# Kernel optimization log

Hardware: AMD Instinct MI355X
Metric: run time of the kernel (lower is better)

The kernel has to match this reference:

```python
import jax, jax.numpy as jnp
import numpy as np

EMBED_DIM = 768
NUM_HEADS = 12
LORA_DIM = 64
HEAD_DIM = EMBED_DIM // NUM_HEADS
SCALING = float(HEAD_DIM) ** -0.5


def quick_gelu(x):
    return x * jax.nn.sigmoid(1.702 * x)


def setup_inputs() -> dict:
    key = jax.random.key(0)
    ks = jax.random.split(key, 12)
    bsz, tgt_len, E = 128, 197, EMBED_DIM
    x = jax.random.normal(ks[0], (bsz, tgt_len, E), dtype=jnp.float32)
    attn_mask = jnp.zeros((bsz, tgt_len, tgt_len), dtype=jnp.float32)
    top_idx = jax.random.randint(ks[1], (bsz,), 0, tgt_len)
    s = 0.02
    return {
        "x": x,
        "attn_mask": attn_mask,
        "in_proj_weight": jax.random.normal(ks[2], (3 * E, E)) * s,
        "in_proj_bias": jnp.zeros((3 * E,), jnp.float32),
        "out_proj_weight": jax.random.normal(ks[3], (E, E)) * s,
        "out_proj_bias": jnp.zeros((E,), jnp.float32),
        "lora_a": jax.random.normal(ks[4], (LORA_DIM, E)) * s,
        "lora_b": jax.random.normal(ks[5], (3 * E, LORA_DIM)) * s,
        "down_weight": jax.random.normal(ks[6], (LORA_DIM, E)) * s,
        "down_bias": jax.random.normal(ks[7], (LORA_DIM,)) * 1e-6,
        "up_weight": jax.random.normal(ks[8], (E, LORA_DIM)) * s,
        "up_bias": jnp.zeros((E,), jnp.float32),
        "n_f": 16,
        "top_idx": top_idx,
    }


def reference(x, attn_mask, in_proj_weight, in_proj_bias, out_proj_weight,
              out_proj_bias, lora_a, lora_b, down_weight, down_bias,
              up_weight, up_bias, n_f, top_idx):
    bsz, tgt_len, E = x.shape
    H, hd = NUM_HEADS, HEAD_DIM
    b = bsz // n_f

    # fused QKV + LoRA delta
    qkv = x @ in_proj_weight.T + in_proj_bias          # [bsz, L, 3E]
    qkv = qkv + (x @ lora_a.T) @ lora_b.T              # LoRA delta
    qkv = qkv.reshape(bsz, tgt_len, 3, H, hd)
    qkv = jnp.transpose(qkv, (2, 0, 3, 1, 4))          # [3, bsz, H, L, hd]
    q, k, v = qkv[0], qkv[1], qkv[2]

    # gather per-sample CLS query before scaling (matches torch order)
    q_1 = q[jnp.arange(bsz), :, top_idx, :]            # [bsz, H, hd]
    q_1 = jnp.transpose(q_1.reshape(b, n_f, H, hd), (0, 2, 1, 3))  # [b, H, f, hd]

    # frame-local attention
    attn = jnp.einsum('bhqd,bhkd->bhqk', q * SCALING, k) + attn_mask[:, None, :, :]
    attn = jax.nn.softmax(attn, axis=-1)
    xo = jnp.einsum('bhqk,bhkd->bhqd', attn, v)
    xo = jnp.transpose(xo, (0, 2, 1, 3)).reshape(bsz, tgt_len, E)
    xo = xo @ out_proj_weight.T + out_proj_bias        # [bsz, L, E]

    # global CLS attention over all frames' keys/values
    k_g = jnp.transpose(k.reshape(b, n_f, H, tgt_len, hd), (0, 2, 1, 3, 4)).reshape(b, H, n_f * tgt_len, hd)
    v_g = jnp.transpose(v.reshape(b, n_f, H, tgt_len, hd), (0, 2, 1, 3, 4)).reshape(b, H, n_f * tgt_len, hd)
    mask_g = attn_mask[:, -1, :].reshape(b, n_f * tgt_len)  # [b, f*L]

    attn_1 = jnp.einsum('bhfd,bhkd->bhfk', q_1 * SCALING, k_g) + mask_g[:, None, None, :]
    attn_1 = jax.nn.softmax(attn_1, axis=-1)
    x_1 = jnp.einsum('bhfk,bhkd->bhfd', attn_1, v_g)
    x_1 = jnp.transpose(x_1, (0, 2, 1, 3)).reshape(b, n_f, E)
    x_1 = x_1 @ out_proj_weight.T + out_proj_bias      # [b, f, E]

    # adapter on gathered CLS outputs
    x_0 = xo[jnp.arange(bsz), top_idx, :].reshape(b, n_f, E)
    x_0 = quick_gelu(x_0 @ down_weight.T + down_bias)
    x_0 = x_0 @ up_weight.T + up_bias                  # [b, f, E]

    update_cls = (x_0 + x_1).reshape(bsz, E)
    xo = xo.at[jnp.arange(bsz), top_idx, :].set(update_cls)
    return xo
```

## Files before the change

### kernel.cpp

```cpp
#include <hip/hip_runtime.h>
#include <hip/hip_bf16.h>

typedef __attribute__((ext_vector_type(4))) float f32x4;
typedef __attribute__((ext_vector_type(8))) short s16x8;

#define BSZ 128
#define TGT 197
#define EDIM 768
#define NH 12
#define HD 64
#define NF 16
#define M_TOT (BSZ*TGT)
#define QKV_N (3*EDIM)
#define KG (NF*TGT)
#define VSTR 264
#define NSPL 8
#define KSPL 394
#define LSTR 424

__device__ __forceinline__ float b2f(unsigned short u) {
  return __uint_as_float(((unsigned int)u) << 16);
}
__device__ __forceinline__ float bf2f(__hip_bfloat16 b) { return __bfloat162float(b); }
__device__ __forceinline__ __hip_bfloat16 f2bf(float f) { return __float2bfloat16(f); }
__device__ __forceinline__ unsigned int packbf(float a, float b) {
  __hip_bfloat16 x = __float2bfloat16(a), y = __float2bfloat16(b);
  return (unsigned int)*(unsigned short*)&x | ((unsigned int)*(unsigned short*)&y << 16);
}
__device__ __forceinline__ int swz(int t, int c) {
  return t*64 + (c ^ ((((t & 7) ^ ((t >> 3) & 3))) << 3));
}
__device__ __forceinline__ int vswz(int d, int t) {
  return d*VSTR + (t ^ (d & 56));
}

__device__ __forceinline__ void gload_lds16(const void* gsrc, void* ldst) {
  __builtin_amdgcn_global_load_lds(
      (const __attribute__((address_space(1))) unsigned int*)gsrc,
      (__attribute__((address_space(3))) unsigned int*)ldst, 16, 0, 0);
}

struct CvBatch {
  const void* src[7];
  void* dst[7];
  int off8[8];
};

__global__ __launch_bounds__(256) void prep(
    const void* __restrict__ xsrc, const void* __restrict__ msrc,
    __hip_bfloat16* __restrict__ x_c, __hip_bfloat16* __restrict__ mask_c,
    CvBatch cb, int* __restrict__ flag, unsigned int* __restrict__ mznz)
{
  __shared__ float smax[256];
  const int tid = threadIdx.x;
  const unsigned short* xs = (const unsigned short*)xsrc;
  float mx = 0.f;
  for (int j = tid; j < 1024; j += 256) {
    float v = fabsf(b2f(xs[j]));
    mx = (v < 1e30f) ? fmaxf(mx, v) : 1e30f;
  }
  smax[tid] = mx;
  __syncthreads();
  if (tid == 0) {
    float m = 0.f;
    for (int j = 0; j < 256; ++j) m = fmaxf(m, smax[j]);
    smax[0] = (m < 100.f) ? 1.f : 0.f;
    if (blockIdx.x == 0) *flag = (m < 100.f) ? 1 : 0;
  }
  __syncthreads();
  const int isbf = (int)smax[0];

  const int gsz = gridDim.x * 256;
  const int gi = blockIdx.x * 256 + tid;

  {
    const unsigned int* mw = (const unsigned int*)msrc;
    const int nwords = isbf ? (4967552/2) : 4967552;
    const unsigned int am = isbf ? 0x7fff7fffu : 0x7fffffffu;
    unsigned int acc = 0;
    for (int i = gi; i < nwords; i += gsz) acc |= (mw[i] & am);
    if (acc) atomicOr(mznz, 1u);
  }

  {
    const int total = cb.off8[7];
    for (int i = gi; i < total; i += gsz) {
      int s = 0;
      #pragma unroll
      for (int k = 1; k < 7; ++k) s += (i >= cb.off8[k]);
      const int li = i - cb.off8[s];
      if (isbf) {
        ((s16x8*)cb.dst[s])[li] = ((const s16x8*)cb.src[s])[li];
      } else {
        const f32x4* sp = (const f32x4*)cb.src[s];
        f32x4 a = sp[li*2], b = sp[li*2+1];
        s16x8 o;
        #pragma unroll
        for (int j = 0; j < 4; ++j) { __hip_bfloat16 t = f2bf(a[j]); o[j] = *(short*)&t; }
        #pragma unroll
        for (int j = 0; j < 4; ++j) { __hip_bfloat16 t = f2bf(b[j]); o[4+j] = *(short*)&t; }
        ((s16x8*)cb.dst[s])[li] = o;
      }
    }
  }

  if (!isbf) {
    {
      const f32x4* s = (const f32x4*)xsrc;
      s16x8* d = (s16x8*)x_c;
      for (int i = gi; i < 19365888/8; i += gsz) {
        f32x4 a = s[i*2], b = s[i*2+1];
        s16x8 o;
        #pragma unroll
        for (int j = 0; j < 4; ++j) { __hip_bfloat16 t = f2bf(a[j]); o[j] = *(short*)&t; }
        #pragma unroll
        for (int j = 0; j < 4; ++j) { __hip_bfloat16 t = f2bf(b[j]); o[4+j] = *(short*)&t; }
        d[i] = o;
      }
    }
    {
      const f32x4* s = (const f32x4*)msrc;
      s16x8* d = (s16x8*)mask_c;
      for (int i = gi; i < 4967552/8; i += gsz) {
        f32x4 a = s[i*2], b = s[i*2+1];
        s16x8 o;
        #pragma unroll
        for (int j = 0; j < 4; ++j) { __hip_bfloat16 t = f2bf(a[j]); o[j] = *(short*)&t; }
        #pragma unroll
        for (int j = 0; j < 4; ++j) { __hip_bfloat16 t = f2bf(b[j]); o[4+j] = *(short*)&t; }
        d[i] = o;
      }
    }
  }
}

__global__ __launch_bounds__(256) void build_wc(
    const void* __restrict__ W,
    const void* __restrict__ la,
    const void* __restrict__ lb,
    __hip_bfloat16* __restrict__ Wc,
    const int* __restrict__ flag)
{
  __shared__ float lbr[64];
  const int isbf = *flag;
  const int n = blockIdx.x;
  if (threadIdx.x < 64)
    lbr[threadIdx.x] = isbf ? bf2f(((const __hip_bfloat16*)lb)[n*64 + threadIdx.x])
                            : ((const float*)lb)[n*64 + threadIdx.x];
  __syncthreads();
  if (isbf) {
    const __hip_bfloat16* Wb = (const __hip_bfloat16*)W;
    const __hip_bfloat16* lab = (const __hip_bfloat16*)la;
    for (int e = threadIdx.x; e < EDIM; e += 256) {
      float acc = bf2f(Wb[(size_t)n*EDIM + e]);
      for (int r = 0; r < 64; ++r) acc += lbr[r] * bf2f(lab[r*EDIM + e]);
      Wc[(size_t)n*EDIM + e] = f2bf(acc);
    }
  } else {
    const float* Wf = (const float*)W;
    const float* laf = (const float*)la;
    for (int e = threadIdx.x; e < EDIM; e += 256) {
      float acc = Wf[(size_t)n*EDIM + e];
      for (int r = 0; r < 64; ++r) acc += lbr[r] * laf[r*EDIM + e];
      Wc[(size_t)n*EDIM + e] = f2bf(acc);
    }
  }
}

__global__ __launch_bounds__(512) void gemm_bt_8ph(
    const __hip_bfloat16* __restrict__ A,
    const __hip_bfloat16* __restrict__ A_alt,
    const __hip_bfloat16* __restrict__ B,
    const __hip_bfloat16* __restrict__ bias,
    void* __restrict__ C,
    int M, int N, int K, int ntiles,
    const int* __restrict__ flag, int flag_mode)
{
  __shared__ char lds[131072];
  const int tid = threadIdx.x;
  const int wave = tid >> 6, lane = tid & 63;
  const int l16 = lane & 15, kq = lane >> 4;
  const int wr = wave >> 2, wc2 = wave & 3;

  const int nwg = gridDim.x;
  const int bid = blockIdx.x;
  const int qc = nwg >> 3, rc = nwg & 7;
  const int xcd = bid & 7;
  const int wgid = (xcd < rc ? xcd*(qc+1) : rc*(qc+1) + (xcd-rc)*qc) + (bid >> 3);
  const long brow = (long)(wgid / ntiles) * 256;
  const long bcol = (long)(wgid % ntiles) * 256;

  const int isbf = *flag;
  const __hip_bfloat16* Ause = isbf ? A_alt : A;
  const int nkt = K >> 6;

  const int srow = tid >> 3;
  const int schunk = tid & 7;
  const int wuni = wave << 10;

  auto stA = [&](int t, int buf, int issue) {
    int ar = issue*64 + srow;
    int cs = schunk ^ (ar & 7);
    long gr = brow + ar; if (gr > (long)M - 1) gr = M - 1;
    gload_lds16(Ause + gr*(long)K + t*64 + cs*8,
                lds + buf*65536 + issue*8192 + wuni);
  };
  auto stB = [&](int t, int buf, int issue) {
    int br = issue*64 + srow;
    int cs = schunk ^ (br & 7);
    gload_lds16(B + (bcol + br)*(long)K + t*64 + cs*8,
                lds + buf*65536 + 32768 + issue*8192 + wuni);
  };
  auto rdA = [&](int buf, int q, int a, int ks) -> s16x8 {
    int ar = wr*128 + q*32 + a*16 + l16;
    int ch = ks*4 + kq;
    return *(const s16x8*)(lds + buf*65536 + ar*128 + ((ch ^ (ar & 7)) << 4));
  };
  auto rdB = [&](int buf, int ni, int ks) -> s16x8 {
    int br = wc2*64 + ni*16 + l16;
    int ch = ks*4 + kq;
    return *(const s16x8*)(lds + buf*65536 + 32768 + br*128 + ((ch ^ (br & 7)) << 4));
  };

  f32x4 acc[8][4];
  #pragma unroll
  for (int i = 0; i < 8; ++i)
    #pragma unroll
    for (int j = 0; j < 4; ++j) acc[i][j] = (f32x4){0.f,0.f,0.f,0.f};

  stB(0,0,0); stB(0,0,1); stB(0,0,2); stB(0,0,3);
  stA(0,0,0); stA(0,0,2); stA(0,0,1); stA(0,0,3);
  asm volatile("s_waitcnt vmcnt(2)" ::: "memory");
  __builtin_amdgcn_s_barrier();

  for (int t = 0; t < nkt; ++t) {
    const int cur = t & 1, nxt = cur ^ 1;
    const bool pf = (t + 1 < nkt);
    s16x8 bfr[4][2], af[2][2];

    #pragma unroll
    for (int ni = 0; ni < 4; ++ni) { bfr[ni][0] = rdB(cur,ni,0); bfr[ni][1] = rdB(cur,ni,1); }
    af[0][0]=rdA(cur,0,0,0); af[0][1]=rdA(cur,0,0,1);
    af[1][0]=rdA(cur,0,1,0); af[1][1]=rdA(cur,0,1,1);
    if (pf) { stB(t+1,nxt,0); stB(t+1,nxt,1); }
    __builtin_amdgcn_s_barrier();
    asm volatile("s_waitcnt lgkmcnt(0)" ::: "memory");
    __builtin_amdgcn_sched_barrier(0);
    __builtin_amdgcn_s_setprio(1);
    #pragma unroll
    for (int ks = 0; ks < 2; ++ks)
      #pragma unroll
      for (int ni = 0; ni < 4; ++ni) {
        acc[0][ni] = __builtin_amdgcn_mfma_f32_16x16x32_bf16(af[0][ks], bfr[ni][ks], acc[0][ni], 0,0,0);
        acc[1][ni] = __builtin_amdgcn_mfma_f32_16x16x32_bf16(af[1][ks], bfr[ni][ks], acc[1][ni], 0,0,0);
      }
    __builtin_amdgcn_s_setprio(0);

    af[0][0]=rdA(cur,1,0,0); af[0][1]=rdA(cur,1,0,1);
    af[1][0]=rdA(cur,1,1,0); af[1][1]=rdA(cur,1,1,1);
    if (pf) {
      stB(t+1,nxt,2); stB(t+1,nxt,3);
      asm volatile("s_waitcnt vmcnt(4)" ::: "memory");
    } else {
      asm volatile("s_waitcnt vmcnt(0)" ::: "memory");
    }
    __builtin_amdgcn_s_barrier();
    asm volatile("s_waitcnt lgkmcnt(0)" ::: "memory");
    __builtin_amdgcn_sched_barrier(0);
    __builtin_amdgcn_s_setprio(1);
    #pragma unroll
    for (int ks = 0; ks < 2; ++ks)
      #pragma unroll
      for (int ni = 0; ni < 4; ++ni) {
        acc[2][ni] = __builtin_amdgcn_mfma_f32_16x16x32_bf16(af[0][ks], bfr[ni][ks], acc[2][ni], 0,0,0);
        acc[3][ni] = __builtin_amdgcn_mfma_f32_16x16x32_bf16(af[1][ks], bfr[ni][ks], acc[3][ni], 0,0,0);
      }
    __builtin_amdgcn_s_setprio(0);

    af[0][0]=rdA(cur,2,0,0); af[0][1]=rdA(cur,2,0,1);
    af[1][0]=rdA(cur,2,1,0); af[1][1]=rdA(cur,2,1,1);
    if (pf) { stA(t+1,nxt,0); stA(t+1,nxt,2); }
    __builtin_amdgcn_s_barrier();
    asm volatile("s_waitcnt lgkmcnt(0)" ::: "memory");
    __builtin_amdgcn_sched_barrier(0);
    __builtin_amdgcn_s_setprio(1);
    #pragma unroll
    for (int ks = 0; ks < 2; ++ks)
      #pragma unroll
      for (int ni = 0; ni < 4; ++ni) {
        acc[4][ni] = __builtin_amdgcn_mfma_f32_16x16x32_bf16(af[0][ks], bfr[ni][ks], acc[4][ni], 0,0,0);
        acc[5][ni] = __builtin_amdgcn_mfma_f32_16x16x32_bf16(af[1][ks], bfr[ni][ks], acc[5][ni], 0,0,0);
      }
    __builtin_amdgcn_s_setprio(0);

    af[0][0]=rdA(cur,3,0,0); af[0][1]=rdA(cur,3,0,1);
    af[1][0]=rdA(cur,3,1,0); af[1][1]=rdA(cur,3,1,1);
    if (pf) { stA(t+1,nxt,1); stA(t+1,nxt,3); }
    asm volatile("s_waitcnt vmcnt(2)" ::: "memory");
    __builtin_amdgcn_s_barrier();
    asm volatile("s_waitcnt lgkmcnt(0)" ::: "memory");
    __builtin_amdgcn_sched_barrier(0);
    __builtin_amdgcn_s_setprio(1);
    #pragma unroll
    for (int ks = 0; ks < 2; ++ks)
      #pragma unroll
      for (int ni = 0; ni < 4; ++ni) {
        acc[6][ni] = __builtin_amdgcn_mfma_f32_16x16x32_bf16(af[0][ks], bfr[ni][ks], acc[6][ni], 0,0,0);
        acc[7][ni] = __builtin_amdgcn_mfma_f32_16x16x32_bf16(af[1][ks], bfr[ni][ks], acc[7][ni], 0,0,0);
      }
    __builtin_amdgcn_s_setprio(0);
  }

  __builtin_amdgcn_s_barrier();

  const int f32o = flag_mode && (!isbf);
  float bv[4];
  #pragma unroll
  for (int ni = 0; ni < 4; ++ni) bv[ni] = bf2f(bias[bcol + wc2*64 + ni*16 + l16]);
  const int o4 = kq*4;

  if (!f32o) {
    __hip_bfloat16* eb = (__hip_bfloat16*)(lds + wave*2048);
    __hip_bfloat16* Cb = (__hip_bfloat16*)C;
    const int rr = lane >> 3, cg = lane & 7;
    #pragma unroll
    for (int mi = 0; mi < 8; ++mi) {
      #pragma unroll
      for (int ni = 0; ni < 4; ++ni)
        #pragma unroll
        for (int r = 0; r < 4; ++r) {
          const int row16 = o4 + r;
          const int sidx = row16*64 + ((((ni*2 + (l16 >> 3)) ^ (row16 & 7)) << 3) | (l16 & 7));
          eb[sidx] = f2bf(acc[mi][ni][r] + bv[ni]);
        }
      asm volatile("s_waitcnt lgkmcnt(0)" ::: "memory");
      __builtin_amdgcn_sched_barrier(0);
      #pragma unroll
      for (int pass = 0; pass < 2; ++pass) {
        const int row16 = pass*8 + rr;
        const long grow = brow + wr*128 + mi*16 + row16;
        if (grow < M) {
          s16x8 v = *(const s16x8*)(eb + row16*64 + ((cg ^ (row16 & 7)) << 3));
          *(s16x8*)(Cb + grow*(long)N + bcol + wc2*64 + cg*8) = v;
        }
      }
      asm volatile("s_waitcnt lgkmcnt(0)" ::: "memory");
      __builtin_amdgcn_sched_barrier(0);
    }
  } else {
    #pragma unroll
    for (int mi = 0; mi < 8; ++mi)
      #pragma unroll
      for (int ni = 0; ni < 4; ++ni)
        #pragma unroll
        for (int r = 0; r < 4; ++r) {
          const long grow = brow + wr*128 + mi*16 + o4 + r;
          if (grow < M)
            ((float*)C)[grow*(long)N + bcol + wc2*64 + ni*16 + l16] = acc[mi][ni][r] + bv[ni];
        }
  }
}

__global__ __launch_bounds__(256) void attn_fused(
    const __hip_bfloat16* __restrict__ qkv,
    const __hip_bfloat16* __restrict__ mask,
    const __hip_bfloat16* __restrict__ mask_raw,
    const int* __restrict__ flag,
    const unsigned int* __restrict__ mzp,
    __hip_bfloat16* __restrict__ xop)
{
  __shared__ __hip_bfloat16 lVt[64*VSTR];

  const int tid = threadIdx.x;
  const int blk = blockIdx.x;
  const int xcd = blk & 7;
  const int slot = blk >> 3;
  const int ih = xcd * 192 + (slot >> 2);
  const int qt = slot & 3;
  const int h = ih % NH;
  const int i = ih / NH;
  const int q0 = qt * 64;
  const size_t rowbase = (size_t)i * TGT;
  const int wave = tid >> 6, lane = tid & 63;
  const int l16 = lane & 15, kq = lane >> 4;
  const int mz = (*mzp == 0u);
  const __hip_bfloat16* msk = (*flag) ? mask_raw : mask;

  int qr = q0 + wave*16 + l16;
  const int qrc = qr > TGT-1 ? TGT-1 : qr;
  s16x8 qf[2];
  #pragma unroll
  for (int kk = 0; kk < 2; ++kk)
    qf[kk] = *(const s16x8*)(qkv + (rowbase + qrc)*QKV_N + h*HD + kk*32 + kq*8);

  const f32x4 z = {0.f,0.f,0.f,0.f};
  for (int idx = tid; idx < 224*8; idx += 256) {
    int t = idx >> 3, c8 = idx & 7;
    f32x4 vv = z;
    if (t < TGT) vv = *(const f32x4*)(qkv + (rowbase + t)*QKV_N + 2*EDIM + h*HD + c8*8);
    const __hip_bfloat16* pv = (const __hip_bfloat16*)&vv;
    const int tx = t ^ (c8 << 3);
    #pragma unroll
    for (int j = 0; j < 8; ++j)
      lVt[(c8*8 + j)*VSTR + tx] = pv[j];
  }
  __syncthreads();

  f32x4 acc[14];
  #pragma unroll
  for (int nf = 0; nf < 14; ++nf) {
    int trow = nf*16 + l16; if (trow > TGT-1) trow = TGT-1;
    acc[nf] = (f32x4){0.f,0.f,0.f,0.f};
    #pragma unroll
    for (int kk = 0; kk < 2; ++kk) {
      s16x8 kf = *(const s16x8*)(qkv + (rowbase + trow)*QKV_N + EDIM + h*HD + kk*32 + kq*8);
      acc[nf] = __builtin_amdgcn_mfma_f32_16x16x32_bf16(kf, qf[kk], acc[nf], 0, 0, 0);
    }
  }

  float mx = -1e30f;
  #pragma unroll
  for (int nf = 0; nf < 14; ++nf) {
    #pragma unroll
    for (int r = 0; r < 4; ++r) {
      const int t = nf*16 + kq*4 + r;
      float s;
      if (t < TGT) {
        s = acc[nf][r]*0.125f;
        if (!mz) s += bf2f(msk[(rowbase + qrc)*TGT + t]);
      } else s = -1e30f;
      acc[nf][r] = s;
      mx = fmaxf(mx, s);
    }
  }
  mx = fmaxf(mx, __shfl_xor(mx, 16));
  mx = fmaxf(mx, __shfl_xor(mx, 32));

  float rs = 0.f;
  unsigned int pk[14][2];
  #pragma unroll
  for (int nf = 0; nf < 14; ++nf) {
    float p0 = __expf(acc[nf][0] - mx);
    float p1 = __expf(acc[nf][1] - mx);
    float p2 = __expf(acc[nf][2] - mx);
    float p3 = __expf(acc[nf][3] - mx);
    rs += (p0 + p1) + (p2 + p3);
    pk[nf][0] = packbf(p0, p1);
    pk[nf][1] = packbf(p2, p3);
  }
  rs += __shfl_xor(rs, 16);
  rs += __shfl_xor(rs, 32);

  f32x4 oacc[4];
  #pragma unroll
  for (int nf = 0; nf < 4; ++nf) oacc[nf] = (f32x4){0.f,0.f,0.f,0.f};

  const int slbase = l16 + ((kq & 1) << 5);
  #pragma unroll
  for (int kt = 0; kt < 7; ++kt) {
    s16x8 pa;
    #pragma unroll
    for (int jp = 0; jp < 4; ++jp) {
      const int srcLane = slbase + ((jp >> 1) << 4);
      int va = __shfl((int)pk[2*kt][jp & 1], srcLane, 64);
      int vb = __shfl((int)pk[2*kt + 1][jp & 1], srcLane, 64);
      int sel = (kq < 2) ? va : vb;
      pa[2*jp]     = (short)(sel & 0xffff);
      pa[2*jp + 1] = (short)(((unsigned int)sel) >> 16);
    }
    #pragma unroll
    for (int nf = 0; nf < 4; ++nf) {
      s16x8 vf = *(const s16x8*)(lVt + vswz(nf*16 + l16, kt*32 + kq*8));
      oacc[nf] = __builtin_amdgcn_mfma_f32_16x16x32_bf16(pa, vf, oacc[nf], 0, 0, 0);
    }
  }

  #pragma unroll
  for (int r = 0; r < 4; ++r) {
    const float rsrc = __shfl(rs, kq*4 + r, 64);
    const int qw = q0 + wave*16 + kq*4 + r;
    if (qw < TGT) {
      const float inv = 1.0f / rsrc;
      #pragma unroll
      for (int nf = 0; nf < 4; ++nf)
        xop[(rowbase + qw)*(size_t)EDIM + h*HD + nf*16 + l16] = f2bf(oacc[nf][r] * inv);
    }
  }
}

__global__ __launch_bounds__(256) void cls_split(
    const __hip_bfloat16* __restrict__ qkv,
    const __hip_bfloat16* __restrict__ mask,
    const __hip_bfloat16* __restrict__ mask_raw,
    const int* __restrict__ flag,
    const unsigned int* __restrict__ mzp,
    const int* __restrict__ top_idx,
    float* __restrict__ pO,
    float* __restrict__ pm,
    float* __restrict__ pl)
{
  __shared__ __hip_bfloat16 lQ[16*64];
  __shared__ __hip_bfloat16 lS[16*LSTR];
  __shared__ __hip_bfloat16 lV[256*64];
  __shared__ float red[16][17];
  __shared__ float rmax[16];
  __shared__ float rsum[16];

  const int tid = threadIdx.x;
  const int sp = blockIdx.x & 7;
  const int gh = blockIdx.x >> 3;
  const int g = gh / NH;
  const int h = gh % NH;
  const int k0 = sp * KSPL;
  const int wave = tid >> 6, lane = tid & 63;
  const int l16 = lane & 15, kq = lane >> 4, o4 = (lane >> 4) * 4;
  const int mz = (*mzp == 0u);
  const __hip_bfloat16* msk = (*flag) ? mask_raw : mask;

  if (tid < 128) {
    int qi = tid >> 3, c8 = tid & 7;
    int ib = g*NF + qi;
    int top = top_idx[ib];
    f32x4 v = *(const f32x4*)(qkv + ((size_t)ib*TGT + top)*QKV_N + h*HD + c8*8);
    *(f32x4*)(lQ + qi*64 + c8*8) = v;
  }
  __syncthreads();

  s16x8 q8[2];
  #pragma unroll
  for (int kk = 0; kk < 2; ++kk)
    q8[kk] = *(const s16x8*)(lQ + l16*64 + kk*32 + kq*8);

  for (int nf = wave; nf < 26; nf += 4) {
    const int keyl = nf*16 + l16;
    const int keyg = k0 + (keyl < KSPL ? keyl : 0);
    f32x4 a = {0.f,0.f,0.f,0.f};
    const size_t krow = (size_t)g*KG + keyg;
    #pragma unroll
    for (int kk = 0; kk < 2; ++kk) {
      s16x8 k8 = *(const s16x8*)(qkv + krow*QKV_N + EDIM + h*HD + kk*32 + kq*8);
      a = __builtin_amdgcn_mfma_f32_16x16x32_bf16(q8[kk], k8, a, 0, 0, 0);
    }
    float mval = 0.f;
    if (!mz && keyl < KSPL) {
      const int f = keyg / 197;
      const int t = keyg - f*197;
      mval = bf2f(msk[((size_t)(g*NF + f)*TGT + (TGT-1))*TGT + t]);
    }
    #pragma unroll
    for (int r = 0; r < 4; ++r)
      lS[(o4 + r)*LSTR + nf*16 + l16] = f2bf(keyl < KSPL ? a[r]*0.125f + mval : -1e30f);
  }
  __syncthreads();

  {
    const int q = tid >> 4, c = tid & 15;
    float mx = -1e30f;
    for (int gch = c; gch < 52; gch += 16) {
      s16x8 sv = *(const s16x8*)(lS + q*LSTR + gch*8);
      #pragma unroll
      for (int j = 0; j < 8; ++j) mx = fmaxf(mx, b2f((unsigned short)sv[j]));
    }
    red[q][c] = mx;
    __syncthreads();
    if (tid < 16) {
      float m = red[tid][0];
      for (int j = 1; j < 16; ++j) m = fmaxf(m, red[tid][j]);
      rmax[tid] = m;
    }
    __syncthreads();
    const float rowmax = rmax[q];
    float sum = 0.f;
    for (int gch = c; gch < 52; gch += 16) {
      s16x8 sv = *(const s16x8*)(lS + q*LSTR + gch*8);
      s16x8 ov;
      #pragma unroll
      for (int jp = 0; jp < 4; ++jp) {
        float e0 = __expf(b2f((unsigned short)sv[2*jp])   - rowmax);
        float e1 = __expf(b2f((unsigned short)sv[2*jp+1]) - rowmax);
        sum += e0 + e1;
        unsigned int pr = packbf(e0, e1);
        ov[2*jp]   = (short)(pr & 0xffff);
        ov[2*jp+1] = (short)(pr >> 16);
      }
      *(s16x8*)(lS + q*LSTR + gch*8) = ov;
    }
    red[q][c] = sum;
    __syncthreads();
    if (tid < 16) {
      float s = 0.f;
      for (int j = 0; j < 16; ++j) s += red[tid][j];
      rsum[tid] = s;
    }
  }

  f32x4 oa = {0.f,0.f,0.f,0.f};
  const f32x4 z = {0.f,0.f,0.f,0.f};
  #pragma unroll
  for (int cki = 0; cki < 2; ++cki) {
    const int ck = cki * 256;
    const int nrows = cki ? 160 : 256;
    const int nks = cki ? 5 : 8;
    __syncthreads();
    for (int idx = tid; idx < nrows*8; idx += 256) {
      int t2 = idx >> 3, c8 = idx & 7;
      int keyl = ck + t2;
      f32x4 v = z;
      if (keyl < KSPL)
        v = *(const f32x4*)(qkv + ((size_t)g*KG + k0 + keyl)*QKV_N + 2*EDIM + h*HD + c8*8);
      *(f32x4*)(lV + swz(t2, c8*8)) = v;
    }
    __syncthreads();
    for (int ks = 0; ks < nks; ++ks) {
      s16x8 pa = *(const s16x8*)(lS + l16*LSTR + ck + ks*32 + kq*8);
      s16x8 vf;
      #pragma unroll
      for (int j = 0; j < 8; ++j) {
        const int t2 = ks*32 + kq*8 + j;
        vf[j] = *(const short*)(lV + swz(t2, wave*16 + l16));
      }
      oa = __builtin_amdgcn_mfma_f32_16x16x32_bf16(pa, vf, oa, 0, 0, 0);
    }
  }

  const int ps = gh*NSPL + sp;
  #pragma unroll
  for (int r = 0; r < 4; ++r)
    pO[((size_t)ps*16 + (o4 + r))*64 + wave*16 + l16] = oa[r];
  if (tid < 16) {
    pm[ps*16 + tid] = rmax[tid];
    pl[ps*16 + tid] = rsum[tid];
  }
}

__global__ __launch_bounds__(256) void cls_combine(
    const float* __restrict__ pO,
    const float* __restrict__ pm,
    const float* __restrict__ pl,
    __hip_bfloat16* __restrict__ x1buf)
{
  __shared__ float M[16];
  __shared__ float L[16];
  __shared__ float sc[NSPL][16];
  const int tid = threadIdx.x;
  const int gh = blockIdx.x;
  const int g = gh / NH;
  const int h = gh % NH;

  if (tid < 16) {
    float m = -1e30f;
    for (int s = 0; s < NSPL; ++s) m = fmaxf(m, pm[(gh*NSPL + s)*16 + tid]);
    M[tid] = m;
  }
  __syncthreads();
  if (tid < 128) {
    const int s = tid >> 4, q = tid & 15;
    sc[s][q] = __expf(pm[(gh*NSPL + s)*16 + q] - M[q]);
  }
  __syncthreads();
  if (tid < 16) {
    float l = 0.f;
    for (int s = 0; s < NSPL; ++s) l += pl[(gh*NSPL + s)*16 + tid] * sc[s][tid];
    L[tid] = l;
  }
  __syncthreads();
  for (int idx = tid; idx < 16*64; idx += 256) {
    const int q = idx >> 6, d = idx & 63;
    float acc = 0.f;
    for (int s = 0; s < NSPL; ++s)
      acc += pO[((size_t)(gh*NSPL + s)*16 + q)*64 + d] * sc[s][q];
    x1buf[((size_t)(g*NF + q))*EDIM + h*64 + d] = f2bf(acc / L[q]);
  }
}

__global__ __launch_bounds__(256) void final_update(
    void* __restrict__ out,
    const __hip_bfloat16* __restrict__ x1p,
    const __hip_bfloat16* __restrict__ dw, const __hip_bfloat16* __restrict__ db,
    const __hip_bfloat16* __restrict__ uw, const __hip_bfloat16* __restrict__ ub,
    const int* __restrict__ top_idx, const int* __restrict__ flag)
{
  __shared__ float x0[EDIM];
  __shared__ float hmid[64];
  const int i = blockIdx.x;
  const int tid = threadIdx.x;
  const int top = top_idx[i];
  const int isbf = *flag;
  const size_t rowoff = ((size_t)i*TGT + top)*EDIM;
  for (int e = tid; e < EDIM; e += 256)
    x0[e] = isbf ? bf2f(((const __hip_bfloat16*)out)[rowoff + e])
                 : ((const float*)out)[rowoff + e];
  __syncthreads();
  if (tid < 64) {
    float a = bf2f(db[tid]);
    for (int e = 0; e < EDIM; ++e) a += x0[e] * bf2f(dw[tid*EDIM + e]);
    hmid[tid] = a / (1.f + __expf(-1.702f * a));
  }
  __syncthreads();
  for (int e = tid; e < EDIM; e += 256) {
    float a = bf2f(ub[e]) + bf2f(x1p[(size_t)i*EDIM + e]);
    #pragma unroll
    for (int r = 0; r < 64; ++r) a += hmid[r] * bf2f(uw[e*64 + r]);
    if (isbf) ((__hip_bfloat16*)out)[rowoff + e] = f2bf(a);
    else ((float*)out)[rowoff + e] = a;
  }
}

extern "C" void kernel_launch(void* const* d_in, const int* in_sizes, int n_in,
                              void* d_out, int out_size, void* d_ws, size_t ws_size,
                              hipStream_t stream) {
  (void)in_sizes; (void)n_in; (void)out_size; (void)ws_size;
  const int* top_idx = (const int*)d_in[13];
  const __hip_bfloat16* x_raw    = (const __hip_bfloat16*)d_in[0];
  const __hip_bfloat16* mask_raw = (const __hip_bfloat16*)d_in[1];

  char* ws = (char*)d_ws;
  size_t off = 0;
  auto alloc = [&](size_t bytes) { char* p = ws + off; off += (bytes + 15) & ~(size_t)15; return p; };

  int* flag = (int*)alloc(16);
  unsigned int* mznz = (unsigned int*)alloc(16);
  __hip_bfloat16* x_c    = (__hip_bfloat16*)alloc((size_t)19365888*2);
  __hip_bfloat16* mask_c = (__hip_bfloat16*)alloc((size_t)4967552*2);
  __hip_bfloat16* bIn_c  = (__hip_bfloat16*)alloc((size_t)2304*2);
  __hip_bfloat16* wOut_c = (__hip_bfloat16*)alloc((size_t)589824*2);
  __hip_bfloat16* bOut_c = (__hip_bfloat16*)alloc((size_t)768*2);
  __hip_bfloat16* dw_c   = (__hip_bfloat16*)alloc((size_t)49152*2);
  __hip_bfloat16* db_c   = (__hip_bfloat16*)alloc((size_t)64*2);
  __hip_bfloat16* uw_c   = (__hip_bfloat16*)alloc((size_t)49152*2);
  __hip_bfloat16* ub_c   = (__hip_bfloat16*)alloc((size_t)768*2);
  __hip_bfloat16* Wc     = (__hip_bfloat16*)alloc((size_t)QKV_N*EDIM*2);
  __hip_bfloat16* qkv    = (__hip_bfloat16*)alloc((size_t)M_TOT*QKV_N*2);
  __hip_bfloat16* xop    = (__hip_bfloat16*)alloc((size_t)M_TOT*EDIM*2);
  __hip_bfloat16* x1b    = (__hip_bfloat16*)alloc((size_t)BSZ*EDIM*2);
  __hip_bfloat16* x1p    = (__hip_bfloat16*)alloc((size_t)BSZ*EDIM*2);
  float* pO = (float*)alloc((size_t)96*NSPL*16*64*4);
  float* pm = (float*)alloc((size_t)96*NSPL*16*4);
  float* pl = (float*)alloc((size_t)96*NSPL*16*4);

  hipMemsetAsync(mznz, 0, 4, stream);

  CvBatch cb;
  const int srcIdx[7] = {3, 4, 5, 8, 9, 10, 11};
  void* dsts[7] = {bIn_c, wOut_c, bOut_c, dw_c, db_c, uw_c, ub_c};
  const int ns[7] = {2304, 589824, 768, 49152, 64, 49152, 768};
  int cum = 0;
  for (int k = 0; k < 7; ++k) {
    cb.src[k] = d_in[srcIdx[k]];
    cb.dst[k] = dsts[k];
    cb.off8[k] = cum;
    cum += ns[k] / 8;
  }
  cb.off8[7] = cum;

  prep<<<2048, 256, 0, stream>>>(d_in[0], d_in[1], x_c, mask_c, cb, flag, mznz);
  build_wc<<<2304, 256, 0, stream>>>(d_in[2], d_in[6], d_in[7], Wc, flag);

  gemm_bt_8ph<<<99*9, 512, 0, stream>>>(x_c, x_raw, Wc, bIn_c, qkv,
                                        M_TOT, QKV_N, EDIM, 9, flag, 0);
  attn_fused<<<dim3(6144), 256, 0, stream>>>(qkv, mask_c, mask_raw, flag, mznz, xop);
  cls_split<<<dim3(96*NSPL), 256, 0, stream>>>(qkv, mask_c, mask_raw, flag, mznz,
                                               top_idx, pO, pm, pl);
  gemm_bt_8ph<<<99*3, 512, 0, stream>>>(xop, xop, wOut_c, bOut_c, d_out,
                                        M_TOT, EDIM, EDIM, 3, flag, 1);
  cls_combine<<<dim3(96), 256, 0, stream>>>(pO, pm, pl, x1b);
  gemm_bt_8ph<<<3, 512, 0, stream>>>(x1b, x1b, wOut_c, bOut_c, x1p,
                                     BSZ, EDIM, EDIM, 3, flag, 0);
  final_update<<<128, 256, 0, stream>>>(d_out, x1p, dw_c, db_c, uw_c, ub_c, top_idx, flag);
}
```

Baseline: 484.4 us.

## Fuse CLS split-softmax combine and out-projection into the final adapter kernel

New measurement: 526.8 us. +8.8%, slower.

```diff
diff --git a/kernel.cpp b/kernel.cpp
--- a/kernel.cpp
+++ b/kernel.cpp
@@ -633,72 +633,64 @@
   }
 }
 
-__global__ __launch_bounds__(256) void cls_combine(
+__global__ __launch_bounds__(256) void final_cls(
+    void* __restrict__ out,
     const float* __restrict__ pO,
     const float* __restrict__ pm,
     const float* __restrict__ pl,
-    __hip_bfloat16* __restrict__ x1buf)
-{
-  __shared__ float M[16];
-  __shared__ float L[16];
-  __shared__ float sc[NSPL][16];
-  const int tid = threadIdx.x;
-  const int gh = blockIdx.x;
-  const int g = gh / NH;
-  const int h = gh % NH;
-
-  if (tid < 16) {
-    float m = -1e30f;
-    for (int s = 0; s < NSPL; ++s) m = fmaxf(m, pm[(gh*NSPL + s)*16 + tid]);
-    M[tid] = m;
-  }
-  __syncthreads();
-  if (tid < 128) {
-    const int s = tid >> 4, q = tid & 15;
-    sc[s][q] = __expf(pm[(gh*NSPL + s)*16 + q] - M[q]);
-  }
-  __syncthreads();
-  if (tid < 16) {
-    float l = 0.f;
-    for (int s = 0; s < NSPL; ++s) l += pl[(gh*NSPL + s)*16 + tid] * sc[s][tid];
-    L[tid] = l;
-  }
-  __syncthreads();
-  for (int idx = tid; idx < 16*64; idx += 256) {
-    const int q = idx >> 6, d = idx & 63;
-    float acc = 0.f;
-    for (int s = 0; s < NSPL; ++s)
-      acc += pO[((size_t)(gh*NSPL + s)*16 + q)*64 + d] * sc[s][q];
-    x1buf[((size_t)(g*NF + q))*EDIM + h*64 + d] = f2bf(acc / L[q]);
-  }
-}
-
-__global__ __launch_bounds__(256) void final_update(
-    void* __restrict__ out,
-    const __hip_bfloat16* __restrict__ x1p,
+    const __hip_bfloat16* __restrict__ wOut,
+    const __hip_bfloat16* __restrict__ bOut,
     const __hip_bfloat16* __restrict__ dw, const __hip_bfloat16* __restrict__ db,
     const __hip_bfloat16* __restrict__ uw, const __hip_bfloat16* __restrict__ ub,
     const int* __restrict__ top_idx, const int* __restrict__ flag)
 {
+  __shared__ float xr[EDIM];
   __shared__ float x0[EDIM];
   __shared__ float hmid[64];
   const int i = blockIdx.x;
   const int tid = threadIdx.x;
+  const int q = i & (NF - 1);
+  const int g = i >> 4;
   const int top = top_idx[i];
   const int isbf = *flag;
   const size_t rowoff = ((size_t)i*TGT + top)*EDIM;
+
+  for (int e = tid; e < EDIM; e += 256) {
+    const int h = e >> 6, d = e & 63;
+    const int gh = g*NH + h;
+    float M = -1e30f;
+    #pragma unroll
+    for (int s = 0; s < NSPL; ++s) M = fmaxf(M, pm[(gh*NSPL + s)*16 + q]);
+    float L = 0.f, acc = 0.f;
+    #pragma unroll
+    for (int s = 0; s < NSPL; ++s) {
+      const float sc = __expf(pm[(gh*NSPL + s)*16 + q] - M);
+      L += pl[(gh*NSPL + s)*16 + q] * sc;
+      acc += pO[((size_t)(gh*NSPL + s)*16 + q)*64 + d] * sc;
+    }
+    xr[e] = acc / L;
+  }
   for (int e = tid; e < EDIM; e += 256)
     x0[e] = isbf ? bf2f(((const __hip_bfloat16*)out)[rowoff + e])
                  : ((const float*)out)[rowoff + e];
   __syncthreads();
+
   if (tid < 64) {
     float a = bf2f(db[tid]);
     for (int e = 0; e < EDIM; ++e) a += x0[e] * bf2f(dw[tid*EDIM + e]);
     hmid[tid] = a / (1.f + __expf(-1.702f * a));
   }
   __syncthreads();
+
   for (int e = tid; e < EDIM; e += 256) {
-    float a = bf2f(ub[e]) + bf2f(x1p[(size_t)i*EDIM + e]);
+    float a = bf2f(bOut[e]);
+    const __hip_bfloat16* wrow = wOut + (size_t)e*EDIM;
+    for (int k8 = 0; k8 < EDIM/8; ++k8) {
+      s16x8 w = *(const s16x8*)(wrow + k8*8);
+      #pragma unroll
+      for (int j = 0; j < 8; ++j) a += xr[k8*8 + j] * b2f((unsigned short)w[j]);
+    }
+    a += bf2f(ub[e]);
     #pragma unroll
     for (int r = 0; r < 64; ++r) a += hmid[r] * bf2f(uw[e*64 + r]);
     if (isbf) ((__hip_bfloat16*)out)[rowoff + e] = f2bf(a);
@@ -732,8 +724,6 @@
   __hip_bfloat16* Wc     = (__hip_bfloat16*)alloc((size_t)QKV_N*EDIM*2);
   __hip_bfloat16* qkv    = (__hip_bfloat16*)alloc((size_t)M_TOT*QKV_N*2);
   __hip_bfloat16* xop    = (__hip_bfloat16*)alloc((size_t)M_TOT*EDIM*2);
-  __hip_bfloat16* x1b    = (__hip_bfloat16*)alloc((size_t)BSZ*EDIM*2);
-  __hip_bfloat16* x1p    = (__hip_bfloat16*)alloc((size_t)BSZ*EDIM*2);
   float* pO = (float*)alloc((size_t)96*NSPL*16*64*4);
   float* pm = (float*)alloc((size_t)96*NSPL*16*4);
   float* pl = (float*)alloc((size_t)96*NSPL*16*4);
@@ -763,8 +753,6 @@
                                                top_idx, pO, pm, pl);
   gemm_bt_8ph<<<99*3, 512, 0, stream>>>(xop, xop, wOut_c, bOut_c, d_out,
                                         M_TOT, EDIM, EDIM, 3, flag, 1);
-  cls_combine<<<dim3(96), 256, 0, stream>>>(pO, pm, pl, x1b);
-  gemm_bt_8ph<<<3, 512, 0, stream>>>(x1b, x1b, wOut_c, bOut_c, x1p,
-                                     BSZ, EDIM, EDIM, 3, flag, 0);
-  final_update<<<128, 256, 0, stream>>>(d_out, x1p, dw_c, db_c, uw_c, ub_c, top_idx, flag);
-}
+  final_cls<<<128, 256, 0, stream>>>(d_out, pO, pm, pl, wOut_c, bOut_c,
+                                     dw_c, db_c, uw_c, ub_c, top_idx, flag);
+}
```
